# Performance work log

Measured on AMD Instinct MI355X. Metric: run time of the kernel, lower is better.

Reference implementation:

```python
import jax, jax.numpy as jnp
import numpy as np

N_EMBD = 1024
N_HEAD = 16
HEAD_DIM = N_EMBD // N_HEAD
EPS = 1e-5


def setup_inputs() -> dict:
    key = jax.random.key(0)
    ks = jax.random.split(key, 12)
    C = N_EMBD
    s = lambda fan_in: 1.0 / np.sqrt(fan_in)
    return {
        "x": jax.random.normal(ks[0], (2, 2048, C), dtype=jnp.float32),
        "ln1_g": jnp.ones((C,), jnp.float32),
        "ln1_b": jnp.zeros((C,), jnp.float32),
        "w_attn": jax.random.normal(ks[1], (C, 3 * C), jnp.float32) * s(C),
        "b_attn": jnp.zeros((3 * C,), jnp.float32),
        "w_proj": jax.random.normal(ks[2], (C, C), jnp.float32) * s(C),
        "b_proj": jnp.zeros((C,), jnp.float32),
        "ln2_g": jnp.ones((C,), jnp.float32),
        "ln2_b": jnp.zeros((C,), jnp.float32),
        "w_fc": jax.random.normal(ks[3], (C, 4 * C), jnp.float32) * s(C),
        "b_fc": jnp.zeros((4 * C,), jnp.float32),
        "w_fc2": jax.random.normal(ks[4], (4 * C, C), jnp.float32) * s(4 * C),
        "b_fc2": jnp.zeros((C,), jnp.float32),
    }


def _layernorm(x, g, b):
    mu = jnp.mean(x, axis=-1, keepdims=True)
    var = jnp.mean(jnp.square(x - mu), axis=-1, keepdims=True)
    return (x - mu) * jax.lax.rsqrt(var + EPS) * g + b


def _attention(x, w_attn, b_attn, w_proj, b_proj):
    B, T, C = x.shape
    qkv = x @ w_attn + b_attn  # [B,T,3C]
    q, k, v = jnp.split(qkv, 3, axis=-1)
    # [B,H,T,D]
    reshape = lambda t: t.reshape(B, T, N_HEAD, HEAD_DIM).transpose(0, 2, 1, 3)
    q, k, v = reshape(q), reshape(k), reshape(v)
    scale = HEAD_DIM ** (-0.5)
    att = jnp.einsum("bhqd,bhkd->bhqk", q, k) * scale  # [B,H,T,T]
    mask = jnp.tril(jnp.ones((T, T), dtype=bool))
    att = jnp.where(mask, att, -jnp.inf)
    att = jax.nn.softmax(att, axis=-1)
    y = jnp.einsum("bhqk,bhkd->bhqd", att, v)
    y = y.transpose(0, 2, 1, 3).reshape(B, T, C)
    return y @ w_proj + b_proj


def _mlp(x, w_fc, b_fc, w_fc2, b_fc2):
    h = jax.nn.gelu(x @ w_fc + b_fc, approximate=False)  # nn.GELU default = exact erf
    return h @ w_fc2 + b_fc2


def reference(x, ln1_g, ln1_b, w_attn, b_attn, w_proj, b_proj,
              ln2_g, ln2_b, w_fc, b_fc, w_fc2, b_fc2):
    x = x + _attention(_layernorm(x, ln1_g, ln1_b), w_attn, b_attn, w_proj, b_proj)
    x = x + _mlp(_layernorm(x, ln2_g, ln2_b), w_fc, b_fc, w_fc2, b_fc2)
    return x
```

## Files before the change

kernel.cpp:

```cpp
#include <hip/hip_runtime.h>
#include <hip/hip_bf16.h>
#include <math.h>

typedef __attribute__((ext_vector_type(8))) __bf16 bf16x8;
typedef __attribute__((ext_vector_type(4))) float floatx4;
typedef __attribute__((ext_vector_type(8))) unsigned short ushort8;

#define C_EMBD 1024
#define T_SEQ 2048
#define NH 16
#define HD 64

#define WAITV(N) asm volatile("s_waitcnt vmcnt(" #N ")" ::: "memory")
#define WAITL(N) asm volatile("s_waitcnt lgkmcnt(" #N ")" ::: "memory")
#define DSR(d, a, OFF) \
  asm volatile("ds_read_b128 %0, %1 offset:" #OFF : "=v"(d) : "v"(a))

static __device__ __forceinline__ unsigned short f2b(float f) {
  __hip_bfloat16 h = __float2bfloat16(f);
  unsigned short u;
  __builtin_memcpy(&u, &h, sizeof(u));
  return u;
}
static __device__ __forceinline__ float b2f(unsigned short u) {
  unsigned int b = ((unsigned int)u) << 16;
  float f;
  __builtin_memcpy(&f, &b, sizeof(f));
  return f;
}

static __device__ __forceinline__ void gload16(const void* g, void* l) {
  __builtin_amdgcn_global_load_lds(
      (__attribute__((address_space(1))) void*)(void*)g,
      (__attribute__((address_space(3))) void*)l, 16, 0, 0);
}

static __device__ __forceinline__ floatx4 mfma_bf16(bf16x8 a, bf16x8 b, floatx4 c) {
  return __builtin_amdgcn_mfma_f32_16x16x32_bf16(a, b, c, 0, 0, 0);
}

static __device__ __forceinline__ unsigned int lds_addr(const void* p) {
  return (unsigned int)(size_t)(__attribute__((address_space(3))) void*)(void*)p;
}

__global__ __launch_bounds__(256) void wtrans(const float* __restrict__ in,
                                              unsigned short* __restrict__ out,
                                              int K, int N) {
  __shared__ float t[32][33];
  int n0 = blockIdx.x * 32, k0 = blockIdx.y * 32;
  int tx = threadIdx.x & 31, ty = threadIdx.x >> 5;
#pragma unroll
  for (int i = 0; i < 4; i++)
    t[ty + i * 8][tx] = in[(size_t)(k0 + ty + i * 8) * N + n0 + tx];
  __syncthreads();
#pragma unroll
  for (int i = 0; i < 4; i++)
    out[(size_t)(n0 + ty + i * 8) * K + k0 + tx] = f2b(t[tx][ty + i * 8]);
}

__global__ __launch_bounds__(256) void ln_fwd(const float* __restrict__ x,
                                              const float* __restrict__ g,
                                              const float* __restrict__ bta,
                                              unsigned short* __restrict__ out) {
  int row = blockIdx.x;
  int t = threadIdx.x;
  const float4* xr = (const float4*)(x + (size_t)row * C_EMBD);
  float4 v = xr[t];
  float s = v.x + v.y + v.z + v.w;
  float ss = v.x * v.x + v.y * v.y + v.z * v.z + v.w * v.w;
#pragma unroll
  for (int m = 1; m < 64; m <<= 1) {
    s += __shfl_xor(s, m, 64);
    ss += __shfl_xor(ss, m, 64);
  }
  __shared__ float ps[8];
  int wv = t >> 6;
  if ((t & 63) == 0) { ps[wv] = s; ps[4 + wv] = ss; }
  __syncthreads();
  s = ps[0] + ps[1] + ps[2] + ps[3];
  ss = ps[4] + ps[5] + ps[6] + ps[7];
  float mu = s * (1.0f / C_EMBD);
  float var = ss * (1.0f / C_EMBD) - mu * mu;
  float rs = rsqrtf(var + 1e-5f);
  float4 gv = ((const float4*)g)[t];
  float4 bv = ((const float4*)bta)[t];
  ushort4 o;
  o.x = f2b((v.x - mu) * rs * gv.x + bv.x);
  o.y = f2b((v.y - mu) * rs * gv.y + bv.y);
  o.z = f2b((v.z - mu) * rs * gv.z + bv.z);
  o.w = f2b((v.w - mu) * rs * gv.w + bv.w);
  *(ushort4*)(out + (size_t)row * C_EMBD + t * 4) = o;
}

template <int EP>
__global__ __launch_bounds__(256, 2) void gemm128(
    const unsigned short* __restrict__ A, const unsigned short* __restrict__ Bt,
    const float* __restrict__ bias, const float* __restrict__ res,
    void* __restrict__ outv, unsigned short* __restrict__ vt,
    float* __restrict__ p0, float* __restrict__ p12,
    int M, int N, int ldK, int KCH) {
  __shared__ __align__(16) unsigned short As[2][8192];
  __shared__ __align__(16) unsigned short Bs[2][8192];
  const int tid = threadIdx.x;
  const int wv = tid >> 6, ln = tid & 63;
  const int quad = ln >> 4, l15 = ln & 15;
  const int wm = wv >> 1, wn = wv & 1;

  const int gx = gridDim.x;
  const int nwg = gx * gridDim.y;
  int id = blockIdx.y * gx + blockIdx.x;
  const int cpx = nwg >> 3;
  id = (id & 7) * cpx + (id >> 3);
  const int n0 = (id % gx) * 128;
  const int m0 = (id / gx) * 128;
  const int bz = blockIdx.z;

  A += (size_t)bz * KCH;
  Bt += (size_t)bz * KCH;

  const unsigned short* aSt =
      A + (size_t)(m0 + wv * 8 + (ln >> 3)) * ldK + (((ln & 7) ^ (ln >> 3)) * 8);
  const unsigned short* bSt =
      Bt + (size_t)(n0 + wv * 8 + (ln >> 3)) * ldK + (((ln & 7) ^ (ln >> 3)) * 8);
  const size_t gstep = (size_t)32 * ldK;

  const int sw0 = ((quad) ^ (l15 & 7)) * 16;
  const int sw1 = ((4 + quad) ^ (l15 & 7)) * 16;
  const unsigned int aoff0 = lds_addr(&As[0][0]) + (wm * 64 + l15) * 128 + sw0;
  const unsigned int aoff1 = lds_addr(&As[0][0]) + (wm * 64 + l15) * 128 + sw1;
  const unsigned int boff0 = lds_addr(&Bs[0][0]) + (wn * 64 + l15) * 128 + sw0;
  const unsigned int boff1 = lds_addr(&Bs[0][0]) + (wn * 64 + l15) * 128 + sw1;

  floatx4 acc[4][4];
#pragma unroll
  for (int i = 0; i < 4; i++)
#pragma unroll
    for (int j = 0; j < 4; j++) acc[i][j] = (floatx4)0.0f;

  const int NT = KCH >> 6;

  auto stA1 = [&](int bi, int kt, int g) {
    gload16(aSt + (size_t)kt * 64 + (size_t)g * gstep,
            &As[bi][(g * 32 + wv * 8) * 64]);
  };
  auto stB1 = [&](int bi, int kt, int g) {
    gload16(bSt + (size_t)kt * 64 + (size_t)g * gstep,
            &Bs[bi][(g * 32 + wv * 8) * 64]);
  };

  stB1(0, 0, 0); stB1(0, 0, 1); stB1(0, 0, 2); stB1(0, 0, 3);
  stA1(0, 0, 0); stA1(0, 0, 1); stA1(0, 0, 2); stA1(0, 0, 3);

  for (int t = 0; t < NT; ++t) {
    const int cur = t & 1;
    const bool more = (t + 1 < NT);
    const unsigned int ab0 = aoff0 + (cur << 14), ab1 = aoff1 + (cur << 14);
    const unsigned int bb0 = boff0 + (cur << 14), bb1 = boff1 + (cur << 14);

    WAITV(0);
    __builtin_amdgcn_s_barrier();

    bf16x8 bf0[4], bf1[4], a0, a1, a2, a3;
    DSR(bf0[0], bb0, 0);    DSR(bf0[1], bb0, 2048);
    DSR(bf0[2], bb0, 4096); DSR(bf0[3], bb0, 6144);
    DSR(bf1[0], bb1, 0);    DSR(bf1[1], bb1, 2048);
    DSR(bf1[2], bb1, 4096); DSR(bf1[3], bb1, 6144);
    DSR(a0, ab0, 0); DSR(a1, ab0, 2048);
    DSR(a2, ab1, 0); DSR(a3, ab1, 2048);
    if (more) {
      stB1(cur ^ 1, t + 1, 0); stB1(cur ^ 1, t + 1, 1);
      stB1(cur ^ 1, t + 1, 2); stB1(cur ^ 1, t + 1, 3);
      stA1(cur ^ 1, t + 1, 0); stA1(cur ^ 1, t + 1, 1);
      stA1(cur ^ 1, t + 1, 2); stA1(cur ^ 1, t + 1, 3);
    }
    WAITL(0);
    __builtin_amdgcn_sched_barrier(0);
    __builtin_amdgcn_s_setprio(1);
#pragma unroll
    for (int ni = 0; ni < 4; ni++) {
      acc[0][ni] = mfma_bf16(a0, bf0[ni], acc[0][ni]);
      acc[0][ni] = mfma_bf16(a2, bf1[ni], acc[0][ni]);
      acc[1][ni] = mfma_bf16(a1, bf0[ni], acc[1][ni]);
      acc[1][ni] = mfma_bf16(a3, bf1[ni], acc[1][ni]);
    }
    __builtin_amdgcn_s_setprio(0);

    DSR(a0, ab0, 4096); DSR(a1, ab0, 6144);
    DSR(a2, ab1, 4096); DSR(a3, ab1, 6144);
    WAITL(0);
    __builtin_amdgcn_sched_barrier(0);
    __builtin_amdgcn_s_setprio(1);
#pragma unroll
    for (int ni = 0; ni < 4; ni++) {
      acc[2][ni] = mfma_bf16(a0, bf0[ni], acc[2][ni]);
      acc[2][ni] = mfma_bf16(a2, bf1[ni], acc[2][ni]);
      acc[3][ni] = mfma_bf16(a1, bf0[ni], acc[3][ni]);
      acc[3][ni] = mfma_bf16(a3, bf1[ni], acc[3][ni]);
    }
    __builtin_amdgcn_s_setprio(0);
  }

#pragma unroll
  for (int mi = 0; mi < 4; mi++) {
#pragma unroll
    for (int ni = 0; ni < 4; ni++) {
      const int col = n0 + wn * 64 + ni * 16 + l15;
      const int rowb = m0 + wm * 64 + mi * 16 + quad * 4;
      const float bc = bias ? bias[col] : 0.0f;
      if (EP == 1) {
#pragma unroll
        for (int r = 0; r < 4; r++) {
          size_t idx = (size_t)(rowb + r) * N + col;
          ((float*)outv)[idx] = acc[mi][ni][r] + bc + res[idx];
        }
      } else if (EP == 2) {
#pragma unroll
        for (int r = 0; r < 4; r++) {
          float v = acc[mi][ni][r] + bc;
          v = 0.5f * v * (1.0f + erff(v * 0.70710678118f));
          ((unsigned short*)outv)[(size_t)(rowb + r) * N + col] = f2b(v);
        }
      } else if (EP == 3) {
        if (col < 2048) {
#pragma unroll
          for (int r = 0; r < 4; r++)
            ((unsigned short*)outv)[(size_t)(rowb + r) * N + col] =
                f2b(acc[mi][ni][r] + bc);
        } else {
          int dall = col - 2048;
          int hh2 = dall >> 6, dd = dall & 63;
          int bq = rowb >> 11, t0 = rowb & 2047;
          __align__(8) unsigned short pk[4];
#pragma unroll
          for (int r = 0; r < 4; r++) pk[r] = f2b(acc[mi][ni][r] + bc);
          *(ushort4*)&vt[(size_t)((bq * NH + hh2) * HD + dd) * T_SEQ + t0] =
              *(const ushort4*)pk;
        }
      } else {
        if (bz == 3) {
#pragma unroll
          for (int r = 0; r < 4; r++) {
            size_t idx = (size_t)(rowb + r) * N + col;
            ((float*)outv)[idx] = acc[mi][ni][r] + bc + res[idx];
          }
        } else {
          const size_t MN = (size_t)M * N;
          float* pp = (bz == 0) ? p0 : p12 + (size_t)(bz - 1) * MN;
#pragma unroll
          for (int r = 0; r < 4; r++)
            pp[(size_t)(rowb + r) * N + col] = acc[mi][ni][r];
        }
      }
    }
  }
}

__global__ __launch_bounds__(256) void red3(const float* __restrict__ p0,
                                            const float* __restrict__ p12,
                                            float* __restrict__ out) {
  const size_t MN4 = (size_t)4096 * 1024 / 4;
  for (size_t i = (size_t)blockIdx.x * 256 + threadIdx.x; i < MN4;
       i += (size_t)gridDim.x * 256) {
    float4 a = ((const float4*)p0)[i];
    float4 b = ((const float4*)p12)[i];
    float4 c = ((const float4*)p12)[i + MN4];
    float4 o = ((float4*)out)[i];
    o.x += a.x + b.x + c.x;
    o.y += a.y + b.y + c.y;
    o.z += a.z + b.z + c.z;
    o.w += a.w + b.w + c.w;
    ((float4*)out)[i] = o;
  }
}

__global__ __launch_bounds__(256) void attn_fwd(const unsigned short* __restrict__ qkv,
                                                const unsigned short* __restrict__ vt,
                                                unsigned short* __restrict__ y) {
  __shared__ __align__(16) unsigned short Ks[3][64 * 64];
  __shared__ __align__(16) unsigned short Vs[3][64 * 64];
  __shared__ __align__(16) unsigned short Ps[4 * 16 * 72];
  const int tid = threadIdx.x;
  const int wv = tid >> 6, ln = tid & 63;
  const int quad = ln >> 4, l15 = ln & 15;
  const int pair = blockIdx.x, h = blockIdx.y, b = blockIdx.z;
  unsigned short* Pw = &Ps[wv * 16 * 72];

  const unsigned short* kbase = qkv + (size_t)b * T_SEQ * 3072 + 1024 + h * HD;
  const unsigned short* vbase = vt + (size_t)(b * NH + h) * HD * T_SEQ;

  int koffs[2], voffs[2], ldst[2];
#pragma unroll
  for (int g = 0; g < 2; g++) {
    int S = wv * 128 + g * 64 + ln;
    int r = S >> 3;
    int c = (S & 7) ^ (r & 7);
    koffs[g] = r * 3072 + c * 8;
    voffs[g] = r * T_SEQ + c * 8;
    ldst[g] = wv * 1024 + g * 512;
  }

  auto stage = [&](int kt, int slot) {
#pragma unroll
    for (int g = 0; g < 2; g++) {
      gload16(kbase + (size_t)(kt * 64) * 3072 + koffs[g], &Ks[slot][ldst[g]]);
      gload16(vbase + kt * 64 + voffs[g], &Vs[slot][ldst[g]]);
    }
  };

  for (int ph = 0; ph < 2; ++ph) {
    const int qt = ph ? (31 - pair) : pair;
    const unsigned short* qp =
        qkv + (size_t)(b * T_SEQ + qt * 64 + wv * 16 + l15) * 3072 + h * HD;
    bf16x8 qf[2];
#pragma unroll
    for (int kc = 0; kc < 2; kc++) {
      ushort8 u = *(const ushort8*)(qp + kc * 32 + quad * 8);
      union { ushort8 u; bf16x8 v; } cv;
#pragma unroll
      for (int j = 0; j < 8; j++) cv.u[j] = f2b(b2f(u[j]) * 0.18033688f);
      qf[kc] = cv.v;
    }

    floatx4 o[4];
#pragma unroll
    for (int dt = 0; dt < 4; dt++) o[dt] = (floatx4)0.0f;
    float lacc = 0.0f;

    stage(0, 0);
    if (qt >= 1) stage(1, 1);

    for (int kt = 0; kt <= qt; ++kt) {
      const int slot = kt % 3;
      const bool diag = (kt == qt);
      if (kt < qt) WAITV(4); else WAITV(0);
      __builtin_amdgcn_s_barrier();
      if (kt + 2 <= qt) stage(kt + 2, (kt + 2) % 3);

      const unsigned short* Kc = Ks[slot];
      const unsigned short* Vc = Vs[slot];
      floatx4 s[4];
#pragma unroll
      for (int nt = 0; nt < 4; nt++) s[nt] = (floatx4)0.0f;
#pragma unroll
      for (int nt = 0; nt < 4; nt++)
#pragma unroll
        for (int kc = 0; kc < 2; kc++) {
          bf16x8 kf = *(const bf16x8*)
              &Kc[(nt * 16 + l15) * 64 + (((kc * 4 + quad) ^ (l15 & 7)) * 8)];
          s[nt] = mfma_bf16(kf, qf[kc], s[nt]);
        }

      float psum = 0.0f;
#pragma unroll
      for (int nt = 0; nt < 4; nt++) {
        __align__(8) unsigned short pk[4];
#pragma unroll
        for (int r = 0; r < 4; r++) {
          float sv = s[nt][r];
          if (diag && (nt * 16 + quad * 4 + r > wv * 16 + l15)) sv = -1e30f;
          float p = exp2f(sv - 12.0f);
          psum += p;
          pk[r] = f2b(p);
        }
        *(ushort4*)&Pw[l15 * 72 + nt * 16 + quad * 4] = *(const ushort4*)pk;
      }
      lacc += psum;

      bf16x8 pf0 = *(const bf16x8*)&Pw[l15 * 72 + quad * 8];
      bf16x8 pf1 = *(const bf16x8*)&Pw[l15 * 72 + 32 + quad * 8];
#pragma unroll
      for (int dt = 0; dt < 4; dt++) {
        bf16x8 vf0 = *(const bf16x8*)
            &Vc[(dt * 16 + l15) * 64 + ((quad ^ (l15 & 7)) * 8)];
        bf16x8 vf1 = *(const bf16x8*)
            &Vc[(dt * 16 + l15) * 64 + (((4 + quad) ^ (l15 & 7)) * 8)];
        o[dt] = mfma_bf16(vf0, pf0, o[dt]);
        o[dt] = mfma_bf16(vf1, pf1, o[dt]);
      }
    }

    lacc += __shfl_xor(lacc, 16, 64);
    lacc += __shfl_xor(lacc, 32, 64);
    float rinv = 1.0f / lacc;
#pragma unroll
    for (int dt = 0; dt < 4; dt++) {
      __align__(8) unsigned short ov[4];
#pragma unroll
      for (int r = 0; r < 4; r++) ov[r] = f2b(o[dt][r] * rinv);
      *(ushort4*)&y[(size_t)(b * T_SEQ + qt * 64 + wv * 16 + l15) * C_EMBD +
                    h * HD + dt * 16 + quad * 4] = *(const ushort4*)ov;
    }
  }
}

extern "C" void kernel_launch(void* const* d_in, const int* in_sizes, int n_in,
                              void* d_out, int out_size, void* d_ws, size_t ws_size,
                              hipStream_t stream) {
  (void)in_sizes; (void)n_in; (void)out_size; (void)ws_size;
  const float* x      = (const float*)d_in[0];
  const float* ln1_g  = (const float*)d_in[1];
  const float* ln1_b  = (const float*)d_in[2];
  const float* w_attn = (const float*)d_in[3];
  const float* b_attn = (const float*)d_in[4];
  const float* w_proj = (const float*)d_in[5];
  const float* b_proj = (const float*)d_in[6];
  const float* ln2_g  = (const float*)d_in[7];
  const float* ln2_b  = (const float*)d_in[8];
  const float* w_fc   = (const float*)d_in[9];
  const float* b_fc   = (const float*)d_in[10];
  const float* w_fc2  = (const float*)d_in[11];
  const float* b_fc2  = (const float*)d_in[12];
  float* out = (float*)d_out;

  char* wsb = (char*)d_ws;
  char* ws = wsb;
  unsigned short* wat  = (unsigned short*)ws; ws += (size_t)3072 * 1024 * 2;
  unsigned short* wpt  = (unsigned short*)ws; ws += (size_t)1024 * 1024 * 2;
  unsigned short* wft  = (unsigned short*)ws; ws += (size_t)4096 * 1024 * 2;
  unsigned short* wf2t = (unsigned short*)ws; ws += (size_t)1024 * 4096 * 2;
  unsigned short* xn   = (unsigned short*)ws; ws += (size_t)4096 * 1024 * 2;
  unsigned short* qkv  = (unsigned short*)ws; ws += (size_t)4096 * 3072 * 2;
  unsigned short* yat  = (unsigned short*)ws; ws += (size_t)4096 * 1024 * 2;
  unsigned short* hbuf = (unsigned short*)ws; ws += (size_t)4096 * 4096 * 2;
  unsigned short* vt = hbuf;
  float* p0  = (float*)wsb;
  float* p12 = (float*)(wsb + (size_t)24 * 1024 * 1024);

  wtrans<<<dim3(3072 / 32, 1024 / 32), 256, 0, stream>>>(w_attn, wat, 1024, 3072);
  wtrans<<<dim3(1024 / 32, 1024 / 32), 256, 0, stream>>>(w_proj, wpt, 1024, 1024);
  wtrans<<<dim3(4096 / 32, 1024 / 32), 256, 0, stream>>>(w_fc, wft, 1024, 4096);
  wtrans<<<dim3(1024 / 32, 4096 / 32), 256, 0, stream>>>(w_fc2, wf2t, 4096, 1024);

  ln_fwd<<<4096, 256, 0, stream>>>(x, ln1_g, ln1_b, xn);
  gemm128<3><<<dim3(3072 / 128, 4096 / 128), 256, 0, stream>>>(
      xn, wat, b_attn, nullptr, qkv, vt, nullptr, nullptr, 4096, 3072, 1024, 1024);
  attn_fwd<<<dim3(16, NH, 2), 256, 0, stream>>>(qkv, vt, yat);
  gemm128<1><<<dim3(1024 / 128, 4096 / 128), 256, 0, stream>>>(
      yat, wpt, b_proj, x, out, nullptr, nullptr, nullptr, 4096, 1024, 1024, 1024);
  ln_fwd<<<4096, 256, 0, stream>>>(out, ln2_g, ln2_b, xn);
  gemm128<2><<<dim3(4096 / 128, 4096 / 128), 256, 0, stream>>>(
      xn, wft, b_fc, nullptr, hbuf, nullptr, nullptr, nullptr, 4096, 4096, 1024, 1024);
  gemm128<4><<<dim3(1024 / 128, 4096 / 128, 4), 256, 0, stream>>>(
      hbuf, wf2t, b_fc2, out, out, nullptr, p0, p12, 4096, 1024, 4096, 1024);
  red3<<<2048, 256, 0, stream>>>(p0, p12, out);
}
```

Baseline: 367.9 us.

## Switch GEMM to triple-buffered K=32 tiles with three blocks per CU

The GEMM main loop now uses K-steps of 32 instead of 64 and a three-stage LDS ring buffer, prefetching two tiles ahead and waiting only on the older loads. The LDS footprint per block drops from 64KB to 48KB, and launch bounds are raised to allow three blocks per CU. The LDS layout and swizzle are redesigned so that two 32-wide rows pack into one 128-byte line. This aims to hide global load latency and raise occupancy. In exchange it doubles the number of barriers per unit of K work, and it may cause register spills under the tighter occupancy bound.

```diff
diff --git a/kernel.cpp b/kernel.cpp
--- a/kernel.cpp
+++ b/kernel.cpp
@@ -93,14 +93,14 @@
 }
 
 template <int EP>
-__global__ __launch_bounds__(256, 2) void gemm128(
+__global__ __launch_bounds__(256, 3) void gemm128(
     const unsigned short* __restrict__ A, const unsigned short* __restrict__ Bt,
     const float* __restrict__ bias, const float* __restrict__ res,
     void* __restrict__ outv, unsigned short* __restrict__ vt,
     float* __restrict__ p0, float* __restrict__ p12,
     int M, int N, int ldK, int KCH) {
-  __shared__ __align__(16) unsigned short As[2][8192];
-  __shared__ __align__(16) unsigned short Bs[2][8192];
+  __shared__ __align__(16) unsigned short As[3][4096];
+  __shared__ __align__(16) unsigned short Bs[3][4096];
   const int tid = threadIdx.x;
   const int wv = tid >> 6, ln = tid & 63;
   const int quad = ln >> 4, l15 = ln & 15;
@@ -118,18 +118,17 @@
   A += (size_t)bz * KCH;
   Bt += (size_t)bz * KCH;
 
-  const unsigned short* aSt =
-      A + (size_t)(m0 + wv * 8 + (ln >> 3)) * ldK + (((ln & 7) ^ (ln >> 3)) * 8);
-  const unsigned short* bSt =
-      Bt + (size_t)(n0 + wv * 8 + (ln >> 3)) * ldK + (((ln & 7) ^ (ln >> 3)) * 8);
-  const size_t gstep = (size_t)32 * ldK;
-
-  const int sw0 = ((quad) ^ (l15 & 7)) * 16;
-  const int sw1 = ((4 + quad) ^ (l15 & 7)) * 16;
-  const unsigned int aoff0 = lds_addr(&As[0][0]) + (wm * 64 + l15) * 128 + sw0;
-  const unsigned int aoff1 = lds_addr(&As[0][0]) + (wm * 64 + l15) * 128 + sw1;
-  const unsigned int boff0 = lds_addr(&Bs[0][0]) + (wn * 64 + l15) * 128 + sw0;
-  const unsigned int boff1 = lds_addr(&Bs[0][0]) + (wn * 64 + l15) * 128 + sw1;
+  const int sx = (ln & 7) ^ (ln >> 3);
+  const int rlane = 2 * (ln >> 3) + (sx >> 2);
+  const int coff = (sx & 3) * 8;
+  const unsigned short* aSt = A + (size_t)(m0 + rlane) * ldK + coff;
+  const unsigned short* bSt = Bt + (size_t)(n0 + rlane) * ldK + coff;
+
+  const int sX = (((l15 & 1) * 4 + quad) ^ (l15 >> 1)) * 16;
+  const unsigned int aoff =
+      lds_addr(&As[0][0]) + (wm * 32 + (l15 >> 1)) * 128 + sX;
+  const unsigned int boff =
+      lds_addr(&Bs[0][0]) + (wn * 32 + (l15 >> 1)) * 128 + sX;
 
   floatx4 acc[4][4];
 #pragma unroll
@@ -137,67 +136,47 @@
 #pragma unroll
     for (int j = 0; j < 4; j++) acc[i][j] = (floatx4)0.0f;
 
-  const int NT = KCH >> 6;
-
-  auto stA1 = [&](int bi, int kt, int g) {
-    gload16(aSt + (size_t)kt * 64 + (size_t)g * gstep,
-            &As[bi][(g * 32 + wv * 8) * 64]);
+  const int NT = KCH >> 5;
+
+  auto stage = [&](int bi, int kt) {
+#pragma unroll
+    for (int g = 0; g < 2; g++) {
+      gload16(aSt + (size_t)(wv * 32 + g * 16) * ldK + kt * 32,
+              &As[bi][(wv * 16 + g * 8) * 64]);
+      gload16(bSt + (size_t)(wv * 32 + g * 16) * ldK + kt * 32,
+              &Bs[bi][(wv * 16 + g * 8) * 64]);
+    }
   };
-  auto stB1 = [&](int bi, int kt, int g) {
-    gload16(bSt + (size_t)kt * 64 + (size_t)g * gstep,
-            &Bs[bi][(g * 32 + wv * 8) * 64]);
-  };
-
-  stB1(0, 0, 0); stB1(0, 0, 1); stB1(0, 0, 2); stB1(0, 0, 3);
-  stA1(0, 0, 0); stA1(0, 0, 1); stA1(0, 0, 2); stA1(0, 0, 3);
-
+
+  stage(0, 0);
+  stage(1, 1);
+
+  int bcur = 0, bstg = 2;
   for (int t = 0; t < NT; ++t) {
-    const int cur = t & 1;
-    const bool more = (t + 1 < NT);
-    const unsigned int ab0 = aoff0 + (cur << 14), ab1 = aoff1 + (cur << 14);
-    const unsigned int bb0 = boff0 + (cur << 14), bb1 = boff1 + (cur << 14);
-
-    WAITV(0);
+    if (t + 1 < NT) WAITV(4); else WAITV(0);
     __builtin_amdgcn_s_barrier();
-
-    bf16x8 bf0[4], bf1[4], a0, a1, a2, a3;
-    DSR(bf0[0], bb0, 0);    DSR(bf0[1], bb0, 2048);
-    DSR(bf0[2], bb0, 4096); DSR(bf0[3], bb0, 6144);
-    DSR(bf1[0], bb1, 0);    DSR(bf1[1], bb1, 2048);
-    DSR(bf1[2], bb1, 4096); DSR(bf1[3], bb1, 6144);
-    DSR(a0, ab0, 0); DSR(a1, ab0, 2048);
-    DSR(a2, ab1, 0); DSR(a3, ab1, 2048);
-    if (more) {
-      stB1(cur ^ 1, t + 1, 0); stB1(cur ^ 1, t + 1, 1);
-      stB1(cur ^ 1, t + 1, 2); stB1(cur ^ 1, t + 1, 3);
-      stA1(cur ^ 1, t + 1, 0); stA1(cur ^ 1, t + 1, 1);
-      stA1(cur ^ 1, t + 1, 2); stA1(cur ^ 1, t + 1, 3);
-    }
+    if (t + 2 < NT) stage(bstg, t + 2);
+
+    const unsigned int ab = aoff + bcur * 8192;
+    const unsigned int bb = boff + bcur * 8192;
+    bf16x8 a0, a1, a2, a3, b0, b1, b2, b3;
+    DSR(b0, bb, 0); DSR(b1, bb, 1024); DSR(b2, bb, 2048); DSR(b3, bb, 3072);
+    DSR(a0, ab, 0); DSR(a1, ab, 1024); DSR(a2, ab, 2048); DSR(a3, ab, 3072);
     WAITL(0);
     __builtin_amdgcn_sched_barrier(0);
     __builtin_amdgcn_s_setprio(1);
 #pragma unroll
     for (int ni = 0; ni < 4; ni++) {
-      acc[0][ni] = mfma_bf16(a0, bf0[ni], acc[0][ni]);
-      acc[0][ni] = mfma_bf16(a2, bf1[ni], acc[0][ni]);
-      acc[1][ni] = mfma_bf16(a1, bf0[ni], acc[1][ni]);
-      acc[1][ni] = mfma_bf16(a3, bf1[ni], acc[1][ni]);
+      bf16x8 bf = (ni == 0) ? b0 : (ni == 1) ? b1 : (ni == 2) ? b2 : b3;
+      acc[0][ni] = mfma_bf16(a0, bf, acc[0][ni]);
+      acc[1][ni] = mfma_bf16(a1, bf, acc[1][ni]);
+      acc[2][ni] = mfma_bf16(a2, bf, acc[2][ni]);
+      acc[3][ni] = mfma_bf16(a3, bf, acc[3][ni]);
     }
     __builtin_amdgcn_s_setprio(0);
 
-    DSR(a0, ab0, 4096); DSR(a1, ab0, 6144);
-    DSR(a2, ab1, 4096); DSR(a3, ab1, 6144);
-    WAITL(0);
-    __builtin_amdgcn_sched_barrier(0);
-    __builtin_amdgcn_s_setprio(1);
-#pragma unroll
-    for (int ni = 0; ni < 4; ni++) {
-      acc[2][ni] = mfma_bf16(a0, bf0[ni], acc[2][ni]);
-      acc[2][ni] = mfma_bf16(a2, bf1[ni], acc[2][ni]);
-      acc[3][ni] = mfma_bf16(a1, bf0[ni], acc[3][ni]);
-      acc[3][ni] = mfma_bf16(a3, bf1[ni], acc[3][ni]);
-    }
-    __builtin_amdgcn_s_setprio(0);
+    bcur = (bcur == 2) ? 0 : bcur + 1;
+    bstg = (bstg == 2) ? 0 : bstg + 1;
   }
 
 #pragma unroll
```

Measured after the change: 372.2 us. No clear change (+1.2%).
